# Kernel optimization log

Measured on AMD Instinct MI355X. Metric: run time of the kernel, lower is better.

The kernel has to match this reference:

```python
import jax, jax.numpy as jnp
import numpy as np

B, T, C = 2, 2048, 1024
N_HEAD = 16
HEAD_DIM = C // N_HEAD
ROPE_BASE = 10000.0


def setup_inputs() -> dict:
    key = jax.random.key(0)
    ks = jax.random.split(key, 5)
    s = 0.02
    return {
        "x": jax.random.normal(ks[0], (B, T, C), dtype=jnp.float32),
        "Wq": jax.random.normal(ks[1], (C, C), dtype=jnp.float32) * s,
        "Wk": jax.random.normal(ks[2], (C, C), dtype=jnp.float32) * s,
        "Wv": jax.random.normal(ks[3], (C, C), dtype=jnp.float32) * s,
        "Wo": jax.random.normal(ks[4], (C, C), dtype=jnp.float32) * s,
    }


def _rope_cos_sin(seq_len, head_dim, dtype):
    inv_freq = 1.0 / (ROPE_BASE ** (jnp.arange(0, head_dim, 2, dtype=jnp.float32) / head_dim))
    t = jnp.arange(seq_len, dtype=jnp.float32)
    freqs = jnp.einsum("i,j->ij", t, inv_freq)          # [T, head_dim/2]
    emb = jnp.concatenate([freqs, freqs], axis=-1)        # [T, head_dim]
    return jnp.cos(emb).astype(dtype), jnp.sin(emb).astype(dtype)


def _rotate_half(x):
    x1, x2 = jnp.split(x, 2, axis=-1)
    return jnp.concatenate([-x2, x1], axis=-1)


def _mha(x, Wq, Wk, Wv, Wo):
    b, t, c = x.shape
    # torch nn.Linear stores weight [out, in]: y = x @ W.T
    q = (x @ Wq.T).reshape(b, t, N_HEAD, HEAD_DIM).transpose(0, 2, 1, 3)  # [B,H,T,D]
    k = (x @ Wk.T).reshape(b, t, N_HEAD, HEAD_DIM).transpose(0, 2, 1, 3)
    v = (x @ Wv.T).reshape(b, t, N_HEAD, HEAD_DIM).transpose(0, 2, 1, 3)
    cos, sin = _rope_cos_sin(t, HEAD_DIM, x.dtype)        # [T,D] each, broadcast over B,H
    q = q * cos + _rotate_half(q) * sin
    k = k * cos + _rotate_half(k) * sin
    scale = 1.0 / np.sqrt(HEAD_DIM).astype(np.float32)
    att = jnp.einsum("bhqd,bhkd->bhqk", q, k) * scale     # [B,H,T,T]
    causal = jnp.tril(jnp.ones((t, t), dtype=bool))
    att = jnp.where(causal, att, jnp.finfo(att.dtype).min)
    att = jax.nn.softmax(att, axis=-1)
    y = jnp.einsum("bhqk,bhkd->bhqd", att, v)             # [B,H,T,D]
    y = y.transpose(0, 2, 1, 3).reshape(b, t, c)
    return y @ Wo.T


def reference(x, Wq, Wk, Wv, Wo):
    return _mha(x, Wq, Wk, Wv, Wo)
```

## Files before the change

### kernel.cpp

```cpp
#include <hip/hip_runtime.h>

#define BB 2
#define TT 2048
#define CC 1024
#define NH 16
#define HD 64

typedef __attribute__((ext_vector_type(8))) short bf16x8;
typedef __attribute__((ext_vector_type(4))) float floatx4;
typedef __attribute__((ext_vector_type(16))) float floatx16;

__device__ __forceinline__ unsigned short f2bf(float f) {
    union { float f; unsigned int u; } v; v.f = f;
    unsigned int u = v.u;
    u = (u + 0x7fffu + ((u >> 16) & 1u)) >> 16;
    return (unsigned short)u;
}
__device__ __forceinline__ float bf2f(unsigned short u) {
    return __uint_as_float((unsigned)u << 16);
}

typedef __attribute__((address_space(3))) unsigned char* lds_ptr_t;
typedef const __attribute__((address_space(1))) unsigned char* glob_ptr_t;
__device__ __forceinline__ void gll16(const void* g, void* l) {
    __builtin_amdgcn_global_load_lds((glob_ptr_t)g, (lds_ptr_t)l, 16, 0, 0);
}

__global__ __launch_bounds__(256) void cast_all_k(const float* __restrict__ x,
                                                  const float* __restrict__ wq,
                                                  const float* __restrict__ wk,
                                                  const float* __restrict__ wv,
                                                  const float* __restrict__ wo,
                                                  unsigned short* __restrict__ xb,
                                                  unsigned short* __restrict__ wqkvb,
                                                  unsigned short* __restrict__ wob,
                                                  float2* __restrict__ tabQ,
                                                  float2* __restrict__ tabK) {
    if (blockIdx.x >= 8192) {
        int idx = (blockIdx.x - 8192) * 256 + threadIdx.x;
        int t = idx >> 5, j = idx & 31;
        const float C1 = 0.41524101186092f;
        const float I2PI = 0.15915494309189535f;
        float rev = (float)t * (__builtin_amdgcn_exp2f(-(float)j * C1) * I2PI);
        rev -= floorf(rev);
        float ang = rev * 6.2831853071796f;
        float c = __cosf(ang), s = __sinf(ang);
        const float qs = 0.18033688011112f;
        tabK[idx] = make_float2(c, s);
        tabQ[idx] = make_float2(c * qs, s * qs);
        return;
    }
    int i = blockIdx.x * 256 + threadIdx.x;
    const float* src;
    unsigned short* dst;
    if (i < 1048576) {
        src = x + (size_t)i * 4;
        dst = xb + (size_t)i * 4;
    } else {
        int w   = (i - 1048576) >> 18;
        int off = (i - 1048576) & 262143;
        const float* s0 = (w == 0) ? wq : (w == 1) ? wk : (w == 2) ? wv : wo;
        unsigned short* d0 = (w == 3) ? wob : (wqkvb + (size_t)w * 1048576);
        src = s0 + (size_t)off * 4;
        dst = d0 + (size_t)off * 4;
    }
    float4 v = *(const float4*)src;
    ushort4 o;
    o.x = f2bf(v.x); o.y = f2bf(v.y); o.z = f2bf(v.z); o.w = f2bf(v.w);
    *(ushort4*)dst = o;
}

__global__ __launch_bounds__(256, 2) void gemm_o_k(const unsigned short* __restrict__ A,
                                                   const unsigned short* __restrict__ Bt,
                                                   float* __restrict__ C, int N, int K) {
    __shared__ __align__(16) unsigned short As[128][64];
    __shared__ __align__(16) unsigned short Bs[64][64];
    const int tid  = threadIdx.x;
    const int wave = tid >> 6;
    const int lane = tid & 63;
    const int quad = lane >> 4;
    const int l16  = lane & 15;
    const int sw   = l16 & 7;
    const int wr = (wave >> 1) * 64;
    const int wc = (wave & 1) * 32;
    const int bid = blockIdx.x;
    const int xcd = bid & 7, sl = bid >> 3;
    const int row0 = (xcd * 4 + (sl >> 4)) * 128;
    const int col0 = (sl & 15) * 64;
    const int w8r = wave * 8 + (lane >> 3);
    const int cg  = ((lane & 7) ^ (lane >> 3)) * 8;
    const int cl  = (lane & 7) * 8;

    const unsigned short* Ap = A  + (size_t)(row0 + w8r) * K + cg;
    const unsigned short* Bp = Bt + (size_t)(col0 + w8r) * K + cg;

    floatx4 acc[4][2];
    #pragma unroll
    for (int i = 0; i < 4; i++)
        #pragma unroll
        for (int j = 0; j < 2; j++) acc[i][j] = (floatx4){0.f, 0.f, 0.f, 0.f};

    for (int k0 = 0; k0 < K; k0 += 64) {
        __syncthreads();
        #pragma unroll
        for (int isu = 0; isu < 4; isu++)
            gll16(Ap + (size_t)(isu * 32) * K + k0, &As[isu * 32 + w8r][cl]);
        #pragma unroll
        for (int isu = 0; isu < 2; isu++)
            gll16(Bp + (size_t)(isu * 32) * K + k0, &Bs[isu * 32 + w8r][cl]);
        __syncthreads();
        #pragma unroll
        for (int kk = 0; kk < 2; kk++) {
            bf16x8 af[4], bfr[2];
            #pragma unroll
            for (int i = 0; i < 4; i++)
                af[i]  = *(const bf16x8*)&As[wr + 16 * i + l16][((kk * 4 + quad) ^ sw) * 8];
            #pragma unroll
            for (int j = 0; j < 2; j++)
                bfr[j] = *(const bf16x8*)&Bs[wc + 16 * j + l16][((kk * 4 + quad) ^ sw) * 8];
            #pragma unroll
            for (int i = 0; i < 4; i++)
                #pragma unroll
                for (int j = 0; j < 2; j++)
                    acc[i][j] = __builtin_amdgcn_mfma_f32_16x16x32_bf16(af[i], bfr[j], acc[i][j], 0, 0, 0);
        }
    }

    #pragma unroll
    for (int i = 0; i < 4; i++)
        #pragma unroll
        for (int j = 0; j < 2; j++)
            #pragma unroll
            for (int r = 0; r < 4; r++) {
                int row = row0 + wr + 16 * i + quad * 4 + r;
                int col = col0 + wc + 16 * j + l16;
                C[(size_t)row * N + col] = acc[i][j][r];
            }
}

__global__ __launch_bounds__(256) void gemm_qkv_k(const unsigned short* __restrict__ A,
                                                  const unsigned short* __restrict__ Bt,
                                                  const float2* __restrict__ tabQ,
                                                  const float2* __restrict__ tabK,
                                                  unsigned short* __restrict__ Qb,
                                                  unsigned short* __restrict__ Kb,
                                                  unsigned short* __restrict__ Vb) {
    __shared__ __align__(16) unsigned short SMEM[128 * 128];
    unsigned short (*As)[64] = (unsigned short(*)[64])SMEM;
    unsigned short (*Bs)[64] = (unsigned short(*)[64])(SMEM + 128 * 64);
    unsigned short (*Eb)[128] = (unsigned short(*)[128])SMEM;
    const int K = 1024;
    const int tid  = threadIdx.x;
    const int wave = tid >> 6;
    const int lane = tid & 63;
    const int quad = lane >> 4;
    const int l16  = lane & 15;
    const int sw   = l16 & 7;
    const int wr = (wave >> 1) * 64;
    const int wc = (wave & 1) * 64;
    const int bid = blockIdx.x;
    const int xcd = bid & 7, sl = bid >> 3;
    const int row0 = (xcd * 4 + sl / 24) * 128;
    const int col0 = (sl % 24) * 128;
    const int w8r = wave * 8 + (lane >> 3);
    const int cg  = ((lane & 7) ^ (lane >> 3)) * 8;
    const int cl  = (lane & 7) * 8;

    const unsigned short* Ap = A  + (size_t)(row0 + w8r) * K + cg;
    const unsigned short* Bp = Bt + (size_t)(col0 + w8r) * K + cg;

    floatx4 acc[4][4];
    #pragma unroll
    for (int i = 0; i < 4; i++)
        #pragma unroll
        for (int j = 0; j < 4; j++) acc[i][j] = (floatx4){0.f, 0.f, 0.f, 0.f};

    for (int k0 = 0; k0 < K; k0 += 64) {
        __syncthreads();
        #pragma unroll
        for (int isu = 0; isu < 4; isu++) {
            gll16(Ap + (size_t)(isu * 32) * K + k0, &As[isu * 32 + w8r][cl]);
            gll16(Bp + (size_t)(isu * 32) * K + k0, &Bs[isu * 32 + w8r][cl]);
        }
        __syncthreads();
        #pragma unroll
        for (int kk = 0; kk < 2; kk++) {
            bf16x8 af[4], bfr[4];
            #pragma unroll
            for (int i = 0; i < 4; i++)
                af[i]  = *(const bf16x8*)&As[wr + 16 * i + l16][((kk * 4 + quad) ^ sw) * 8];
            #pragma unroll
            for (int j = 0; j < 4; j++)
                bfr[j] = *(const bf16x8*)&Bs[wc + 16 * j + l16][((kk * 4 + quad) ^ sw) * 8];
            #pragma unroll
            for (int i = 0; i < 4; i++)
                #pragma unroll
                for (int j = 0; j < 4; j++)
                    acc[i][j] = __builtin_amdgcn_mfma_f32_16x16x32_bf16(af[i], bfr[j], acc[i][j], 0, 0, 0);
        }
    }

    __syncthreads();
    #pragma unroll
    for (int i = 0; i < 4; i++)
        #pragma unroll
        for (int j = 0; j < 4; j++)
            #pragma unroll
            for (int r = 0; r < 4; r++) {
                int erow = wr + 16 * i + quad * 4 + r;
                int col  = wc + 16 * j + l16;
                int pcol = (((col >> 3) ^ (erow & 15)) << 3) | (col & 7);
                Eb[erow][pcol] = f2bf(acc[i][j][r]);
            }
    __syncthreads();

    const int row  = tid >> 1;
    const int half = tid & 1;
    const int grow = row0 + row;
    const int t    = grow & (TT - 1);
    const int bb   = grow >> 11;
    const int sect = col0 >> 10;
    const int hh   = ((col0 & 1023) >> 6) + half;
    union { int4 q[8]; unsigned short u[64]; } raw;
    #pragma unroll
    for (int i = 0; i < 8; i++) {
        int pg = (half * 8 + i) ^ (row & 15);
        raw.q[i] = *(const int4*)&Eb[row][pg << 3];
    }
    size_t obase = ((size_t)(bb * NH + hh) * TT + t) * 64;
    if (sect == 2) {
        #pragma unroll
        for (int i = 0; i < 8; i++) *(int4*)(Vb + obase + 8 * i) = raw.q[i];
    } else {
        const float4* tab = (const float4*)((sect ? tabK : tabQ) + (size_t)t * 32);
        unsigned short* dst = sect ? Kb : Qb;
        union { int4 q[8]; unsigned short u[64]; } o;
        #pragma unroll
        for (int i = 0; i < 16; i++) {
            float4 cs = tab[i];
            int j0 = 2 * i, j1 = 2 * i + 1;
            float a0 = bf2f(raw.u[j0]), b0 = bf2f(raw.u[j0 + 32]);
            float a1 = bf2f(raw.u[j1]), b1 = bf2f(raw.u[j1 + 32]);
            o.u[j0]      = f2bf(a0 * cs.x - b0 * cs.y);
            o.u[j0 + 32] = f2bf(b0 * cs.x + a0 * cs.y);
            o.u[j1]      = f2bf(a1 * cs.z - b1 * cs.w);
            o.u[j1 + 32] = f2bf(b1 * cs.z + a1 * cs.w);
        }
        #pragma unroll
        for (int i = 0; i < 8; i++) *(int4*)(dst + obase + 8 * i) = o.q[i];
    }
}

__global__ __launch_bounds__(256) void vtr_k(const unsigned short* __restrict__ Vb,
                                             unsigned short* __restrict__ Vt) {
    __shared__ __align__(16) unsigned short Vsh[64][70];
    const int tid = threadIdx.x;
    const int tt = blockIdx.x;
    const int bh = blockIdx.y;
    const int sr = tid >> 2;
    const int sc = (tid & 3) * 16;
    const unsigned short* src = Vb + ((size_t)bh * TT + tt * 64 + sr) * 64 + sc;
    *(int4*)&Vsh[sr][sc]     = *(const int4*)src;
    *(int4*)&Vsh[sr][sc + 8] = *(const int4*)(src + 8);
    __syncthreads();
    const int dr = tid >> 2;
    const int tc = (tid & 3) * 16;
    unsigned short tv[16];
    #pragma unroll
    for (int i = 0; i < 16; i++) {
        int x = tc + i;
        int key = (x & ~15) + (x & 3) + ((x >> 2) & 1) * 8 + ((x >> 3) & 1) * 4;
        tv[i] = Vsh[key][dr];
    }
    size_t vo = ((size_t)bh * 64 + dr) * TT + tt * 64 + tc;
    *(int4*)(Vt + vo)     = *(int4*)&tv[0];
    *(int4*)(Vt + vo + 8) = *(int4*)&tv[8];
}

__global__ __launch_bounds__(256, 4) void flash_k(const unsigned short* __restrict__ Qb,
                                                  const unsigned short* __restrict__ Kb,
                                                  const unsigned short* __restrict__ Vt,
                                                  unsigned short* __restrict__ Yb) {
    __shared__ __align__(16) unsigned short SMEM[2][2][64][64];
    const int tid  = threadIdx.x;
    const int wave = tid >> 6;
    const int lane = tid & 63;
    const int h    = lane >> 5;
    const int l32  = lane & 31;
    const int g    = wave >> 1;
    const int s    = wave & 1;
    const int j    = blockIdx.x >> 5;
    const int qj   = (j < 16) ? (31 - j) : (j - 16);
    const int bh   = blockIdx.x & 31;
    const int q0   = qj * 64;
    const int qw   = q0 + g * 32 + l32;
    const int nt   = qj + 1;
    const int n0   = (nt + 1) >> 1;
    const int n1   = nt - n0;
    const int l8  = lane >> 3;
    const int lg  = lane & 7;
    const int srow = wave * 8 + l8;
    const int sgr  = lg ^ l8;
    const int xr   = l32 & 7;

    bf16x8 qf[4];
    {
        const unsigned short* qp = Qb + ((size_t)bh * TT + qw) * 64 + h * 8;
        #pragma unroll
        for (int kk = 0; kk < 4; kk++) qf[kk] = *(const bf16x8*)(qp + kk * 16);
    }

    floatx16 accO[2];
    accO[0] = (floatx16)(0.f);
    accO[1] = (floatx16)(0.f);
    float lsum = 0.f;

    const unsigned short* kbase = Kb + (size_t)bh * TT * 64;
    const unsigned short* vbase = Vt + (size_t)bh * 64 * TT;

    for (int i = 0; i < n0; i++) {
        __syncthreads();
        const bool both = (i < n1);
        #pragma unroll
        for (int c = 0; c < 2; c++) {
            int r = 32 * c + srow;
            gll16(kbase + ((size_t)(i * 64) + r) * 64 + sgr * 8, &SMEM[0][0][r][lg * 8]);
        }
        if (both) {
            #pragma unroll
            for (int c = 0; c < 2; c++) {
                int r = 32 * c + srow;
                gll16(kbase + ((size_t)((n0 + i) * 64) + r) * 64 + sgr * 8, &SMEM[0][1][r][lg * 8]);
            }
        }
        #pragma unroll
        for (int c = 0; c < 2; c++) {
            int r = 32 * c + srow;
            gll16(vbase + (size_t)r * TT + i * 64 + sgr * 8, &SMEM[1][0][r][lg * 8]);
        }
        if (both) {
            #pragma unroll
            for (int c = 0; c < 2; c++) {
                int r = 32 * c + srow;
                gll16(vbase + (size_t)r * TT + (n0 + i) * 64 + sgr * 8, &SMEM[1][1][r][lg * 8]);
            }
        }
        if (both) asm volatile("s_waitcnt vmcnt(4)" ::: "memory");
        else      asm volatile("s_waitcnt vmcnt(2)" ::: "memory");
        __builtin_amdgcn_s_barrier();

        const int kt = (s ? n0 : 0) + i;
        const bool active = (s == 0) || both;
        const bool diag = (kt == qj);
        bf16x8 pfrag[4];

        if (active) {
            #pragma unroll
            for (int mb = 0; mb < 2; mb++) {
                floatx16 sacc = (floatx16)(0.f);
                __builtin_amdgcn_s_setprio(1);
                #pragma unroll
                for (int kk = 0; kk < 4; kk++) {
                    bf16x8 kf = *(const bf16x8*)&SMEM[0][s][32 * mb + l32][((2 * kk + h) ^ xr) * 8];
                    sacc = __builtin_amdgcn_mfma_f32_32x32x16_bf16(kf, qf[kk], sacc, 0, 0, 0);
                }
                __builtin_amdgcn_s_setprio(0);
                float p[16];
                const int kmb = kt * 64 + 32 * mb + 4 * h;
                #pragma unroll
                for (int r = 0; r < 16; r++) {
                    float pv = __builtin_amdgcn_exp2f(sacc[r]);
                    if (diag) {
                        int ki = kmb + (r & 3) + 8 * (r >> 2);
                        if (ki > qw) pv = 0.f;
                    }
                    lsum += pv;
                    p[r] = pv;
                }
                #pragma unroll
                for (int half = 0; half < 2; half++) {
                    union { bf16x8 v; unsigned u[4]; } pk;
                    #pragma unroll
                    for (int i2 = 0; i2 < 4; i2++) {
                        unsigned ulo = __float_as_uint(p[half * 8 + 2 * i2]);
                        unsigned uhi = __float_as_uint(p[half * 8 + 2 * i2 + 1]);
                        pk.u[i2] = (ulo >> 16) | (uhi & 0xffff0000u);
                    }
                    pfrag[2 * mb + half] = pk.v;
                }
            }
        }

        asm volatile("s_waitcnt vmcnt(0)" ::: "memory");
        __builtin_amdgcn_s_barrier();

        if (active) {
            __builtin_amdgcn_s_setprio(1);
            #pragma unroll
            for (int mbo = 0; mbo < 2; mbo++) {
                #pragma unroll
                for (int kk = 0; kk < 4; kk++) {
                    bf16x8 vf = *(const bf16x8*)&SMEM[1][s][32 * mbo + l32][((2 * kk + h) ^ xr) * 8];
                    accO[mbo] = __builtin_amdgcn_mfma_f32_32x32x16_bf16(vf, pfrag[kk], accO[mbo], 0, 0, 0);
                }
            }
            __builtin_amdgcn_s_setprio(0);
        }
    }

    lsum += __shfl_xor(lsum, 32);
    __syncthreads();
    float* Fb = (float*)&SMEM[0][0][0][0];
    float* Lb = Fb + 64 * 65;
    if (s == 1) {
        float* f = Fb + (size_t)(g * 32 + l32) * 65;
        #pragma unroll
        for (int mbo = 0; mbo < 2; mbo++)
            #pragma unroll
            for (int a = 0; a < 4; a++) {
                int d0 = 32 * mbo + 8 * a + 4 * h;
                f[d0 + 0] = accO[mbo][4 * a + 0];
                f[d0 + 1] = accO[mbo][4 * a + 1];
                f[d0 + 2] = accO[mbo][4 * a + 2];
                f[d0 + 3] = accO[mbo][4 * a + 3];
            }
        if (lane < 32) Lb[g * 32 + l32] = lsum;
    }
    __syncthreads();
    if (s == 0) {
        const float* f = Fb + (size_t)(g * 32 + l32) * 65;
        const float inv = 1.0f / (lsum + Lb[g * 32 + l32]);
        const int bb = bh >> 4, hh = bh & 15;
        unsigned short* orow = Yb + ((size_t)(bb * TT + qw)) * CC + hh * 64;
        #pragma unroll
        for (int mbo = 0; mbo < 2; mbo++)
            #pragma unroll
            for (int a = 0; a < 4; a++) {
                int d0 = 32 * mbo + 8 * a + 4 * h;
                ushort4 o4;
                o4.x = f2bf((accO[mbo][4 * a + 0] + f[d0 + 0]) * inv);
                o4.y = f2bf((accO[mbo][4 * a + 1] + f[d0 + 1]) * inv);
                o4.z = f2bf((accO[mbo][4 * a + 2] + f[d0 + 2]) * inv);
                o4.w = f2bf((accO[mbo][4 * a + 3] + f[d0 + 3]) * inv);
                *(ushort4*)(orow + d0) = o4;
            }
    }
}

extern "C" void kernel_launch(void* const* d_in, const int* in_sizes, int n_in,
                              void* d_out, int out_size, void* d_ws, size_t ws_size,
                              hipStream_t stream) {
    (void)in_sizes; (void)n_in; (void)out_size; (void)ws_size;
    const float* x  = (const float*)d_in[0];
    const float* Wq = (const float*)d_in[1];
    const float* Wk = (const float*)d_in[2];
    const float* Wv = (const float*)d_in[3];
    const float* Wo = (const float*)d_in[4];
    float* out = (float*)d_out;
    char* ws = (char*)d_ws;

    unsigned short* xb    = (unsigned short*)(ws + 0);
    unsigned short* wqkvb = (unsigned short*)(ws + (8ull  << 20));
    unsigned short* wob   = (unsigned short*)(ws + (14ull << 20));
    unsigned short* Qb    = (unsigned short*)(ws + (16ull << 20));
    unsigned short* Kb    = (unsigned short*)(ws + (24ull << 20));
    unsigned short* Vb    = (unsigned short*)(ws + (32ull << 20));
    unsigned short* Vt    = (unsigned short*)(ws + (40ull << 20));
    unsigned short* Yb    = (unsigned short*)(ws + (48ull << 20));
    float2* tabQ = (float2*)(ws + (73ull << 20));
    float2* tabK = (float2*)(ws + (73ull << 20) + (512ull << 10));

    cast_all_k<<<8448, 256, 0, stream>>>(x, Wq, Wk, Wv, Wo, xb, wqkvb, wob, tabQ, tabK);
    gemm_qkv_k<<<768, 256, 0, stream>>>(xb, wqkvb, tabQ, tabK, Qb, Kb, Vb);
    vtr_k<<<dim3(32, 32), 256, 0, stream>>>(Vb, Vt);
    flash_k<<<1024, 256, 0, stream>>>(Qb, Kb, Vt, Yb);
    gemm_o_k<<<512, 256, 0, stream>>>(Yb, wob, out, 1024, 1024);
}
```

Measured before the change: 169.8 us.

## Fuse V transpose into QKV GEMM epilogue and drop vtr kernel

For the V section, the QKV GEMM epilogue now reads the swizzled LDS tile column-wise and writes V directly in the transposed, key-permuted layout that flash attention expects. The separate vtr_k kernel and the intermediate Vb buffer go away. This removes one launch and a full global write-and-read of V. In exchange, the V blocks do 64 scalar LDS reads per thread, which may cause bank conflicts. A stray unused label was also added in the host launcher.

```diff
diff --git a/kernel.cpp b/kernel.cpp
--- a/kernel.cpp
+++ b/kernel.cpp
@@ -144,7 +144,7 @@
                                                   const float2* __restrict__ tabK,
                                                   unsigned short* __restrict__ Qb,
                                                   unsigned short* __restrict__ Kb,
-                                                  unsigned short* __restrict__ Vb) {
+                                                  unsigned short* __restrict__ Vt) {
     __shared__ __align__(16) unsigned short SMEM[128 * 128];
     unsigned short (*As)[64] = (unsigned short(*)[64])SMEM;
     unsigned short (*Bs)[64] = (unsigned short(*)[64])(SMEM + 128 * 64);
@@ -214,24 +214,37 @@
             }
     __syncthreads();
 
-    const int row  = tid >> 1;
-    const int half = tid & 1;
-    const int grow = row0 + row;
-    const int t    = grow & (TT - 1);
-    const int bb   = grow >> 11;
     const int sect = col0 >> 10;
-    const int hh   = ((col0 & 1023) >> 6) + half;
-    union { int4 q[8]; unsigned short u[64]; } raw;
-    #pragma unroll
-    for (int i = 0; i < 8; i++) {
-        int pg = (half * 8 + i) ^ (row & 15);
-        raw.q[i] = *(const int4*)&Eb[row][pg << 3];
-    }
-    size_t obase = ((size_t)(bb * NH + hh) * TT + t) * 64;
     if (sect == 2) {
-        #pragma unroll
-        for (int i = 0; i < 8; i++) *(int4*)(Vb + obase + 8 * i) = raw.q[i];
+        const int c   = tid >> 1;
+        const int th  = tid & 1;
+        const int hhl = c >> 6, d = c & 63;
+        const int bh2 = (row0 >> 11) * NH + ((col0 & 1023) >> 6) + hhl;
+        const int t0  = (row0 & (TT - 1)) + th * 64;
+        union { int4 q[8]; unsigned short u[64]; } tv;
+        #pragma unroll
+        for (int x = 0; x < 64; x++) {
+            int pr   = (x & ~15) + (x & 3) + ((x >> 2) & 1) * 8 + ((x >> 3) & 1) * 4;
+            int srcr = th * 64 + pr;
+            tv.u[x] = Eb[srcr][(((c >> 3) ^ (srcr & 15)) << 3) | (c & 7)];
+        }
+        unsigned short* vdst = Vt + ((size_t)bh2 * 64 + d) * TT + t0;
+        #pragma unroll
+        for (int i = 0; i < 8; i++) *(int4*)(vdst + 8 * i) = tv.q[i];
     } else {
+        const int row  = tid >> 1;
+        const int half = tid & 1;
+        const int grow = row0 + row;
+        const int t    = grow & (TT - 1);
+        const int bb   = grow >> 11;
+        const int hh   = ((col0 & 1023) >> 6) + half;
+        union { int4 q[8]; unsigned short u[64]; } raw;
+        #pragma unroll
+        for (int i = 0; i < 8; i++) {
+            int pg = (half * 8 + i) ^ (row & 15);
+            raw.q[i] = *(const int4*)&Eb[row][pg << 3];
+        }
+        size_t obase = ((size_t)(bb * NH + hh) * TT + t) * 64;
         const float4* tab = (const float4*)((sect ? tabK : tabQ) + (size_t)t * 32);
         unsigned short* dst = sect ? Kb : Qb;
         union { int4 q[8]; unsigned short u[64]; } o;
@@ -249,32 +262,6 @@
         #pragma unroll
         for (int i = 0; i < 8; i++) *(int4*)(dst + obase + 8 * i) = o.q[i];
     }
-}
-
-__global__ __launch_bounds__(256) void vtr_k(const unsigned short* __restrict__ Vb,
-                                             unsigned short* __restrict__ Vt) {
-    __shared__ __align__(16) unsigned short Vsh[64][70];
-    const int tid = threadIdx.x;
-    const int tt = blockIdx.x;
-    const int bh = blockIdx.y;
-    const int sr = tid >> 2;
-    const int sc = (tid & 3) * 16;
-    const unsigned short* src = Vb + ((size_t)bh * TT + tt * 64 + sr) * 64 + sc;
-    *(int4*)&Vsh[sr][sc]     = *(const int4*)src;
-    *(int4*)&Vsh[sr][sc + 8] = *(const int4*)(src + 8);
-    __syncthreads();
-    const int dr = tid >> 2;
-    const int tc = (tid & 3) * 16;
-    unsigned short tv[16];
-    #pragma unroll
-    for (int i = 0; i < 16; i++) {
-        int x = tc + i;
-        int key = (x & ~15) + (x & 3) + ((x >> 2) & 1) * 8 + ((x >> 3) & 1) * 4;
-        tv[i] = Vsh[key][dr];
-    }
-    size_t vo = ((size_t)bh * 64 + dr) * TT + tt * 64 + tc;
-    *(int4*)(Vt + vo)     = *(int4*)&tv[0];
-    *(int4*)(Vt + vo + 8) = *(int4*)&tv[8];
 }
 
 __global__ __launch_bounds__(256, 4) void flash_k(const unsigned short* __restrict__ Qb,
@@ -464,15 +451,14 @@
     unsigned short* wob   = (unsigned short*)(ws + (14ull << 20));
     unsigned short* Qb    = (unsigned short*)(ws + (16ull << 20));
     unsigned short* Kb    = (unsigned short*)(ws + (24ull << 20));
-    unsigned short* Vb    = (unsigned short*)(ws + (32ull << 20));
     unsigned short* Vt    = (unsigned short*)(ws + (40ull << 20));
     unsigned short* Yb    = (unsigned short*)(ws + (48ull << 20));
     float2* tabQ = (float2*)(ws + (73ull << 20));
     float2* tabK = (float2*)(ws + (73ull << 20) + (512ull << 10));
 
     cast_all_k<<<8448, 256, 0, stream>>>(x, Wq, Wk, Wv, Wo, xb, wqkvb, wob, tabQ, tabK);
-    gemm_qkv_k<<<768, 256, 0, stream>>>(xb, wqkvb, tabQ, tabK, Qb, Kb, Vb);
-    vtr_k<<<dim3(32, 32), 256, 0, stream>>>(Vb, Vt);
+    gemm_qkv_k<<<768, 256, 0, stream>>>(xb, wqkvb, tabQ, tabK, Qb, Kb, Vt);
     flash_k<<<1024, 256, 0, stream>>>(Qb, Kb, Vt, Yb);
+    combine_unused:;
     gemm_o_k<<<512, 256, 0, stream>>>(Yb, wob, out, 1024, 1024);
 }
```

After: 181.5 us. 1.07x slower.

## Prefetch next K tile during PV phase and next V tile after it

Applied to the files above, without the earlier changes.

Moves the K/V global-to-LDS loads out of the top of the attention loop into a prologue plus in-loop prefetches. The next K tile is issued right after the QK-phase barrier so it overlaps the PV MFMAs, and the next V tile is issued after an added barrier following PV. This hides load latency behind compute instead of stalling at the loop start. It drops the leading __syncthreads, adds one barrier per iteration, and relies on the vmcnt counts still matching the reordered loads.

```diff
diff --git a/kernel.cpp b/kernel.cpp
--- a/kernel.cpp
+++ b/kernel.cpp
@@ -318,33 +318,36 @@
     const unsigned short* kbase = Kb + (size_t)bh * TT * 64;
     const unsigned short* vbase = Vt + (size_t)bh * 64 * TT;
 
-    for (int i = 0; i < n0; i++) {
-        __syncthreads();
-        const bool both = (i < n1);
+    {
+        const bool both0 = (0 < n1);
         #pragma unroll
         for (int c = 0; c < 2; c++) {
             int r = 32 * c + srow;
-            gll16(kbase + ((size_t)(i * 64) + r) * 64 + sgr * 8, &SMEM[0][0][r][lg * 8]);
-        }
-        if (both) {
+            gll16(kbase + (size_t)r * 64 + sgr * 8, &SMEM[0][0][r][lg * 8]);
+        }
+        if (both0) {
             #pragma unroll
             for (int c = 0; c < 2; c++) {
                 int r = 32 * c + srow;
-                gll16(kbase + ((size_t)((n0 + i) * 64) + r) * 64 + sgr * 8, &SMEM[0][1][r][lg * 8]);
+                gll16(kbase + ((size_t)(n0 * 64) + r) * 64 + sgr * 8, &SMEM[0][1][r][lg * 8]);
             }
         }
         #pragma unroll
         for (int c = 0; c < 2; c++) {
             int r = 32 * c + srow;
-            gll16(vbase + (size_t)r * TT + i * 64 + sgr * 8, &SMEM[1][0][r][lg * 8]);
-        }
-        if (both) {
+            gll16(vbase + (size_t)r * TT + sgr * 8, &SMEM[1][0][r][lg * 8]);
+        }
+        if (both0) {
             #pragma unroll
             for (int c = 0; c < 2; c++) {
                 int r = 32 * c + srow;
-                gll16(vbase + (size_t)r * TT + (n0 + i) * 64 + sgr * 8, &SMEM[1][1][r][lg * 8]);
-            }
-        }
+                gll16(vbase + (size_t)r * TT + n0 * 64 + sgr * 8, &SMEM[1][1][r][lg * 8]);
+            }
+        }
+    }
+
+    for (int i = 0; i < n0; i++) {
+        const bool both = (i < n1);
         if (both) asm volatile("s_waitcnt vmcnt(4)" ::: "memory");
         else      asm volatile("s_waitcnt vmcnt(2)" ::: "memory");
         __builtin_amdgcn_s_barrier();
@@ -394,6 +397,22 @@
         asm volatile("s_waitcnt vmcnt(0)" ::: "memory");
         __builtin_amdgcn_s_barrier();
 
+        if (i + 1 < n0) {
+            const bool bothn = (i + 1 < n1);
+            #pragma unroll
+            for (int c = 0; c < 2; c++) {
+                int r = 32 * c + srow;
+                gll16(kbase + ((size_t)((i + 1) * 64) + r) * 64 + sgr * 8, &SMEM[0][0][r][lg * 8]);
+            }
+            if (bothn) {
+                #pragma unroll
+                for (int c = 0; c < 2; c++) {
+                    int r = 32 * c + srow;
+                    gll16(kbase + ((size_t)((n0 + i + 1) * 64) + r) * 64 + sgr * 8, &SMEM[0][1][r][lg * 8]);
+                }
+            }
+        }
+
         if (active) {
             __builtin_amdgcn_s_setprio(1);
             #pragma unroll
@@ -405,6 +424,23 @@
                 }
             }
             __builtin_amdgcn_s_setprio(0);
+        }
+
+        __builtin_amdgcn_s_barrier();
+        if (i + 1 < n0) {
+            const bool bothn = (i + 1 < n1);
+            #pragma unroll
+            for (int c = 0; c < 2; c++) {
+                int r = 32 * c + srow;
+                gll16(vbase + (size_t)r * TT + (i + 1) * 64 + sgr * 8, &SMEM[1][0][r][lg * 8]);
+            }
+            if (bothn) {
+                #pragma unroll
+                for (int c = 0; c < 2; c++) {
+                    int r = 32 * c + srow;
+                    gll16(vbase + (size_t)r * TT + (n0 + i + 1) * 64 + sgr * 8, &SMEM[1][1][r][lg * 8]);
+                }
+            }
         }
     }
 
```

After: 166.4 us. -2.0%, faster.
